# Kernel optimization log

Hardware: AMD Instinct MI355X
Metric: run time of the kernel (lower is better)

The kernel has to match this reference:

```python
import jax, jax.numpy as jnp
import numpy as np

NMS_KS = 15
TOP_K = 2048
GAUSS_KS = 7
GAUSS_SIGMA = 1.0
LOSS_LAMBDA = 1.0


def setup_inputs() -> dict:
    key = jax.random.key(0)
    k1, k2, k3 = jax.random.split(key, 3)
    B, H, W = 16, 1024, 1024
    score1 = jax.random.uniform(k1, (B, 1, H, W), dtype=jnp.float32)
    w_score2 = jax.random.uniform(k2, (B, 1, H, W), dtype=jnp.float32)
    w_vis_mask2 = jax.random.randint(k3, (B, 1, H, W), 0, 2) > 0
    return {"score1": score1, "w_score2": w_score2, "w_vis_mask2": w_vis_mask2}


def _nms(score, ks):
    # keep only local maxima within a ks x ks window (stride 1, 'same' padding)
    pooled = jax.lax.reduce_window(score, -jnp.inf, jax.lax.max,
                                   (1, 1, ks, ks), (1, 1, 1, 1), 'SAME')
    return jnp.where(score == pooled, score, jnp.zeros_like(score))


def _prepare_gt_score(score, nms_ks, k, mask):
    # NMS -> mask -> per-image top-k -> binary GT keypoint map
    s = _nms(score, nms_ks) * mask.astype(score.dtype)
    b = s.shape[0]
    flat = s.reshape(b, -1)                      # B x (H*W)
    _, idx = jax.lax.top_k(flat, k)              # B x k
    gt = jnp.zeros_like(flat).at[jnp.arange(b)[:, None], idx].set(1.0)
    return gt.reshape(s.shape)


def _gaussian_filter(x, ks, sigma):
    coords = jnp.arange(ks, dtype=jnp.float32) - (ks - 1) / 2.0
    g = jnp.exp(-(coords ** 2) / (2.0 * sigma ** 2))
    g = g / g.sum()
    k2d = jnp.outer(g, g)[None, None]
    pad = ks // 2
    return jax.lax.conv_general_dilated(
        x, k2d, (1, 1), [(pad, pad), (pad, pad)],
        dimension_numbers=('NCHW', 'OIHW', 'NCHW'))


def reference(score1, w_score2, w_vis_mask2):
    b = score1.shape[0]
    gt_score1 = jax.lax.stop_gradient(
        _prepare_gt_score(w_score2, NMS_KS, TOP_K, w_vis_mask2))
    gt_score1 = _gaussian_filter(gt_score1, GAUSS_KS, GAUSS_SIGMA)
    m = w_vis_mask2.astype(jnp.float32)
    loss = ((score1 - gt_score1) ** 2) * m       # masked elementwise MSE
    loss = loss.reshape(b, -1).sum(-1) / jnp.clip(m.reshape(b, -1).sum(-1), 1e-8)
    return LOSS_LAMBDA * loss.mean()
```

## Files before the change

### kernel.cpp

```cpp
#include <hip/hip_runtime.h>
#include <math.h>

#define BATCH 16
#define H 1024
#define W 1024
#define NTILES 8192
#define NBANDS (NTILES * 4)
#define CAP 4096
#define TOPK 2048
#define BCW 12

struct WS {
  float pt1[NBANDS];
  int   pmc[NBANDS];
  int   band_cnt[NBANDS];
  float corr_part[BATCH * 64];
  float band_val[NBANDS * BCW];
  int   band_idx[NBANDS * BCW];
};

__constant__ float GW[7] = {
  0.004433048175f, 0.054005582623f, 0.242036229376f, 0.399050279652f,
  0.242036229376f, 0.054005582623f, 0.004433048175f
};

__device__ __forceinline__ float4 max4(float4 a, float4 b) {
  float4 r;
  r.x = fmaxf(a.x, b.x); r.y = fmaxf(a.y, b.y);
  r.z = fmaxf(a.z, b.z); r.w = fmaxf(a.w, b.w);
  return r;
}

__global__ __launch_bounds__(256, 5) void k_nms(const float* __restrict__ score1,
                                                const float* __restrict__ score2,
                                                const int* __restrict__ mask,
                                                WS* __restrict__ ws) {
  __shared__ float4 halo[4][22][21];
  const int tid = threadIdx.x;
  const int w = tid >> 6, l = tid & 63;

  const int t = (blockIdx.x & 7) * (NTILES / 8) + (blockIdx.x >> 3);
  const int b  = t >> 9;
  const int tt = t & 511;
  const int ty0 = (tt >> 4) << 5;
  const int tx0 = (tt & 15) << 6;
  const int by0 = ty0 + (w << 3);
  const size_t ibase = (size_t)b * ((size_t)H * W);
  const float* s2 = score2 + ibase;

  const int rl = l >> 3;
  const int c8 = l & 7;
  const size_t pb = ibase + (size_t)(by0 + rl) * W + tx0 + (c8 << 3);
  const float4 s1a = *(const float4*)(score1 + pb);
  const float4 s1b = *(const float4*)(score1 + pb + 4);
  const int4  mka = *(const int4*)(mask + pb);
  const int4  mkb = *(const int4*)(mask + pb + 4);

  float4 st[7]; int sr[7], sc[7];
  #pragma unroll
  for (int k = 0; k < 7; k++) {
    const int slot = l + (k << 6);
    if (slot < 440) {
      const int r = slot / 20, c = slot - r * 20;
      sr[k] = r; sc[k] = c;
      const int gy = by0 - 7 + r, gx = tx0 - 8 + (c << 2);
      const bool ok = (gy >= 0) & (gy < H) & (gx >= 0) & (gx < W);
      const int gyc = min(max(gy, 0), H - 1);
      const int gxc = ok ? gx : 0;
      float4 v = *(const float4*)(s2 + (size_t)gyc * W + gxc);
      if (!ok) v = make_float4(-INFINITY, -INFINITY, -INFINITY, -INFINITY);
      st[k] = v;
    }
  }

  float t1 = 0.f; int mcnt = 0; unsigned int mbits = 0;
  {
    const float sc_[8] = {s1a.x, s1a.y, s1a.z, s1a.w, s1b.x, s1b.y, s1b.z, s1b.w};
    const int   mm[8] = {mka.x, mka.y, mka.z, mka.w, mkb.x, mkb.y, mkb.z, mkb.w};
    #pragma unroll
    for (int j = 0; j < 8; j++) {
      if (mm[j]) { t1 = fmaf(sc_[j], sc_[j], t1); mcnt++; mbits |= (1u << j); }
    }
  }

  #pragma unroll
  for (int k = 0; k < 7; k++) {
    const int slot = l + (k << 6);
    if (slot < 440) halo[w][sr[k]][sc[k]] = st[k];
  }
  __builtin_amdgcn_wave_barrier();
  asm volatile("s_waitcnt lgkmcnt(0)" ::: "memory");
  __builtin_amdgcn_sched_barrier(0);

  float4 vr0, vr1, vr2, vr3;
  int R0 = 0, cg = 0;
  if (l < 40) {
    const int r2 = l / 20;
    cg = l - r2 * 20;
    R0 = r2 << 2;
    float4 core = halo[w][R0 + 3][cg];
    #pragma unroll
    for (int k = 4; k <= 14; k++) core = max4(core, halo[w][R0 + k][cg]);
    const float4 h0 = halo[w][R0][cg], h1 = halo[w][R0 + 1][cg], h2 = halo[w][R0 + 2][cg];
    const float4 h15 = halo[w][R0 + 15][cg], h16 = halo[w][R0 + 16][cg], h17 = halo[w][R0 + 17][cg];
    const float4 p2 = h2, p1 = max4(h1, p2), p0 = max4(h0, p1);
    const float4 sf15 = h15, sf16 = max4(sf15, h16), sf17 = max4(sf16, h17);
    vr0 = max4(core, p0);
    vr1 = max4(max4(core, p1), sf15);
    vr2 = max4(max4(core, p2), sf16);
    vr3 = max4(core, sf17);
  }
  const float4 cva = halo[w][rl + 7][(c8 << 1) + 2];
  const float4 cvb = halo[w][rl + 7][(c8 << 1) + 3];
  __builtin_amdgcn_wave_barrier();
  asm volatile("s_waitcnt lgkmcnt(0)" ::: "memory");
  __builtin_amdgcn_sched_barrier(0);

  if (l < 40) {
    halo[w][R0 + 0][cg] = vr0;
    halo[w][R0 + 1][cg] = vr1;
    halo[w][R0 + 2][cg] = vr2;
    halo[w][R0 + 3][cg] = vr3;
  }
  __builtin_amdgcn_wave_barrier();
  asm volatile("s_waitcnt lgkmcnt(0)" ::: "memory");
  __builtin_amdgcn_sched_barrier(0);

  float r[24];
  #pragma unroll
  for (int g = 0; g < 6; g++) {
    float4 v = halo[w][rl][(c8 << 1) + g];
    r[4 * g + 0] = v.x; r[4 * g + 1] = v.y; r[4 * g + 2] = v.z; r[4 * g + 3] = v.w;
  }
  float core = r[8];
  #pragma unroll
  for (int k = 9; k <= 15; k++) core = fmaxf(core, r[k]);
  const float q7 = r[7];
  const float q6 = fmaxf(r[6], q7);
  const float q5 = fmaxf(r[5], q6);
  const float q4 = fmaxf(r[4], q5);
  const float q3 = fmaxf(r[3], q4);
  const float q2 = fmaxf(r[2], q3);
  const float q1 = fmaxf(r[1], q2);
  float sa[7];
  sa[0] = r[16];
  #pragma unroll
  for (int k = 1; k < 7; k++) sa[k] = fmaxf(sa[k - 1], r[16 + k]);
  float pooled[8];
  pooled[0] = fmaxf(core, q1);
  pooled[1] = fmaxf(fmaxf(core, q2), sa[0]);
  pooled[2] = fmaxf(fmaxf(core, q3), sa[1]);
  pooled[3] = fmaxf(fmaxf(core, q4), sa[2]);
  pooled[4] = fmaxf(fmaxf(core, q5), sa[3]);
  pooled[5] = fmaxf(fmaxf(core, q6), sa[4]);
  pooled[6] = fmaxf(fmaxf(core, q7), sa[5]);
  pooled[7] = fmaxf(core, sa[6]);

  const float cc[8] = {cva.x, cva.y, cva.z, cva.w, cvb.x, cvb.y, cvb.z, cvb.w};
  int cj = -1; float cv = 0.f;
  #pragma unroll
  for (int j = 0; j < 8; j++) {
    if (((mbits >> j) & 1u) && cj < 0) {
      const float s = cc[j];
      if (s == pooled[j] && s > 0.f) { cj = j; cv = s; }
    }
  }
  const int band = (t << 2) + w;
  const unsigned long long bal = __ballot(cj >= 0);
  if (cj >= 0) {
    const int pos = (int)__popcll(bal & ((1ull << l) - 1ull));
    if (pos < BCW) {
      ws->band_val[band * BCW + pos] = cv;
      ws->band_idx[band * BCW + pos] = (by0 + rl) * W + tx0 + (c8 << 3) + cj;
    }
  }
  #pragma unroll
  for (int off = 32; off > 0; off >>= 1) {
    t1 += __shfl_down(t1, off);
    mcnt += __shfl_down(mcnt, off);
  }
  if (l == 0) {
    int nc = (int)__popcll(bal); if (nc > BCW) nc = BCW;
    ws->band_cnt[band] = nc;
    ws->pt1[band] = t1;
    ws->pmc[band] = mcnt;
  }
}

__global__ __launch_bounds__(256, 4) void k_rankstamp(const float* __restrict__ score1,
                                                      const int* __restrict__ mask,
                                                      WS* __restrict__ ws) {
  const int blk = (blockIdx.x & 7) * 128 + (blockIdx.x >> 3);
  const int b = blk >> 6;
  const int slice = blk & 63;
  __shared__ __align__(16) float sval[CAP];
  __shared__ __align__(16) int   sidx[CAP];
  __shared__ int   wt[4];
  __shared__ int   s_tot;
  __shared__ int   s_prank[4][64];
  __shared__ int   s_keys[64];
  __shared__ int   s_nk;
  __shared__ float cred[4];
  const int tid = threadIdx.x;
  const int w = tid >> 6, l = tid & 63;

  const int base = b * 2048 + tid * 8;
  int c[8]; int csum = 0;
  #pragma unroll
  for (int u = 0; u < 8; u++) {
    int x = ws->band_cnt[base + u];
    if (x > BCW) x = BCW;
    c[u] = x; csum += x;
  }
  int v = csum;
  #pragma unroll
  for (int off = 1; off < 64; off <<= 1) {
    int u2 = __shfl_up(v, off);
    if (l >= off) v += u2;
  }
  if (l == 63) wt[w] = v;
  __syncthreads();
  int wo = 0;
  #pragma unroll
  for (int k = 0; k < 4; k++) if (k < w) wo += wt[k];
  const int excl = v - csum + wo;
  if (tid == 255) {
    int tot = excl + csum;
    if (tot > CAP) tot = CAP;
    s_tot = tot;
    #pragma unroll
    for (int u = 0; u < 3; u++)
      if (tot + u < CAP) sval[tot + u] = 0.f;
  }
  int off = excl;
  #pragma unroll
  for (int u = 0; u < 8; u++) {
    const float* sv = ws->band_val + (size_t)(base + u) * BCW;
    const int*   si = ws->band_idx + (size_t)(base + u) * BCW;
    for (int j = 0; j < c[u]; j++) {
      if (off < CAP) { sval[off] = sv[j]; sidx[off] = si[j]; }
      off++;
    }
  }
  __syncthreads();

  const int n = s_tot;
  const int i0 = slice << 6;
  if (i0 >= n) {
    if (tid == 0) ws->corr_part[b * 64 + slice] = 0.f;
    return;
  }
  const int nf4 = (n + 3) >> 2;

  const float vi = sval[i0 + l];
  const int   xi = sidx[i0 + l];
  const int q = (nf4 + 3) >> 2;
  int lo = w * q; if (lo > nf4) lo = nf4;
  int hi = lo + q; if (hi > nf4) hi = nf4;
  int rank = 0;
  int j = lo;
  for (; j + 4 <= hi; j += 4) {
    #pragma unroll
    for (int u = 0; u < 4; u++) {
      const float4 vv = ((const float4*)sval)[j + u];
      const int4  iv = ((const int4*)sidx)[j + u];
      rank += (vv.x > vi) + (vv.y > vi) + (vv.z > vi) + (vv.w > vi);
      rank += (vv.x == vi && iv.x < xi);
      rank += (vv.y == vi && iv.y < xi);
      rank += (vv.z == vi && iv.z < xi);
      rank += (vv.w == vi && iv.w < xi);
    }
  }
  for (; j < hi; j++) {
    const float4 vv = ((const float4*)sval)[j];
    const int4  iv = ((const int4*)sidx)[j];
    rank += (vv.x > vi) + (vv.y > vi) + (vv.z > vi) + (vv.w > vi);
    rank += (vv.x == vi && iv.x < xi);
    rank += (vv.y == vi && iv.y < xi);
    rank += (vv.z == vi && iv.z < xi);
    rank += (vv.w == vi && iv.w < xi);
  }
  s_prank[w][l] = rank;
  __syncthreads();

  if (tid < 64) {
    const int rtot = s_prank[0][tid] + s_prank[1][tid] + s_prank[2][tid] + s_prank[3][tid];
    const bool sel = (i0 + tid < n) && (rtot < TOPK);
    const unsigned long long bal = __ballot(sel);
    if (sel) {
      const int pos = __popcll(bal & ((1ull << tid) - 1ull));
      s_keys[pos] = sidx[i0 + tid];
    }
    if (tid == 0) s_nk = (int)__popcll(bal);
  }
  __syncthreads();
  const int nk = s_nk;

  float contrib = 0.f;
  const int sub = tid & 7;
  const size_t ib2 = (size_t)b * ((size_t)H * W);
  #pragma unroll
  for (int rnd = 0; rnd < 2; rnd++) {
    const int k = (tid >> 3) + (rnd << 5);
    if (k < nk && sub < 7) {
      const int ck = s_keys[k];
      const int cy = ck >> 10, cx = ck & 1023;
      const int py = cy + sub - 3;
      const float wy = GW[sub] * ((py >= 0 && py < H) ? 1.f : 0.f);
      const int pyc = min(max(py, 0), H - 1);
      const float* s1r = score1 + ib2 + (size_t)pyc * W;
      const int*   mr  = mask   + ib2 + (size_t)pyc * W;
      #pragma unroll
      for (int dx = -3; dx <= 3; dx++) {
        const int px = cx + dx;
        const float wv = wy * GW[dx + 3] * ((px >= 0 && px < W) ? 1.f : 0.f);
        const int pxc = min(max(px, 0), W - 1);
        const float mf = (mr[pxc] != 0) ? 1.f : 0.f;
        contrib += mf * wv * (wv - 2.f * s1r[pxc]);
      }
    }
  }
  #pragma unroll
  for (int off2 = 32; off2 > 0; off2 >>= 1) contrib += __shfl_down(contrib, off2);
  if (l == 0) cred[w] = contrib;
  __syncthreads();
  if (tid == 0)
    ws->corr_part[b * 64 + slice] = (cred[0] + cred[1]) + (cred[2] + cred[3]);
}

__global__ __launch_bounds__(1024) void k_final(WS* __restrict__ ws, float* __restrict__ out) {
  const int tid = threadIdx.x;
  const int b = tid >> 6, l = tid & 63;
  __shared__ double sD[BATCH];

  double tsum = 0.0; long long msum = 0;
  const float4* pv = (const float4*)(ws->pt1 + b * 2048);
  const int4*   pm = (const int4*)(ws->pmc + b * 2048);
  #pragma unroll
  for (int k = 0; k < 8; k++) {
    const float4 f = pv[l + (k << 6)];
    const int4   m = pm[l + (k << 6)];
    tsum += (double)f.x + (double)f.y + (double)f.z + (double)f.w;
    msum += (long long)(m.x + m.y + m.z + m.w);
  }
  double csum = (double)ws->corr_part[b * 64 + l];
  #pragma unroll
  for (int off = 32; off > 0; off >>= 1) {
    tsum += __shfl_down(tsum, off);
    msum += __shfl_down(msum, off);
    csum += __shfl_down(csum, off);
  }
  if (l == 0) {
    double denom = (double)msum;
    if (denom < 1e-8) denom = 1e-8;
    sD[b] = (tsum + csum) / denom;
  }
  __syncthreads();
  if (tid == 0) {
    double acc = 0.0;
    #pragma unroll
    for (int k = 0; k < BATCH; k++) acc += sD[k];
    out[0] = (float)(acc / BATCH);
  }
}

extern "C" void kernel_launch(void* const* d_in, const int* in_sizes, int n_in,
                              void* d_out, int out_size, void* d_ws, size_t ws_size,
                              hipStream_t stream) {
  const float* score1 = (const float*)d_in[0];
  const float* score2 = (const float*)d_in[1];
  const int*   mask   = (const int*)d_in[2];
  float* out = (float*)d_out;
  WS* ws = (WS*)d_ws;

  k_nms<<<NTILES, 256, 0, stream>>>(score1, score2, mask, ws);
  k_rankstamp<<<BATCH * 64, 256, 0, stream>>>(score1, mask, ws);
  k_final<<<1, 1024, 0, stream>>>(ws, out);
}
```

Baseline: 89.76 us.

## Compact per-image candidates once in a separate kernel before rank stamping

Moves the band-count prefix scan and scattered candidate gather out of every rank-stamp block into a new per-image compaction kernel that writes a contiguous candidate list to global memory. Each rank-stamp block then checks its slice against the stored count first, exiting early before touching band data, and otherwise loads the compact list with vectorized float4/int4 copies. This removes 64-fold redundant scanning and gathering per image, at the cost of an extra launch, a tiny 16-block kernel, and an extra global round trip.

```diff
diff --git a/kernel.cpp b/kernel.cpp
--- a/kernel.cpp
+++ b/kernel.cpp
@@ -14,9 +14,12 @@
   float pt1[NBANDS];
   int   pmc[NBANDS];
   int   band_cnt[NBANDS];
+  int   cand_count[BATCH];
   float corr_part[BATCH * 64];
   float band_val[NBANDS * BCW];
   int   band_idx[NBANDS * BCW];
+  float ccand_val[BATCH * CAP];
+  int   ccand_idx[BATCH * CAP];
 };
 
 __constant__ float GW[7] = {
@@ -187,70 +190,83 @@
   }
 }
 
+__global__ __launch_bounds__(256) void k_compact(WS* __restrict__ ws) {
+  const int b = blockIdx.x;
+  const int tid = threadIdx.x;
+  const int lane = tid & 63, w = tid >> 6;
+  __shared__ int wt[4];
+
+  const int base = b * 2048 + tid * 8;
+  int c[8]; int csum = 0;
+  #pragma unroll
+  for (int u = 0; u < 8; u++) {
+    int x = ws->band_cnt[base + u];
+    if (x > BCW) x = BCW;
+    c[u] = x; csum += x;
+  }
+  int v = csum;
+  #pragma unroll
+  for (int off = 1; off < 64; off <<= 1) {
+    int u2 = __shfl_up(v, off);
+    if (lane >= off) v += u2;
+  }
+  if (lane == 63) wt[w] = v;
+  __syncthreads();
+  int wo = 0;
+  #pragma unroll
+  for (int k = 0; k < 4; k++) if (k < w) wo += wt[k];
+  const int excl = v - csum + wo;
+  float* dv = ws->ccand_val + b * CAP;
+  int*   di = ws->ccand_idx + b * CAP;
+  if (tid == 255) {
+    int tot = excl + csum;
+    if (tot > CAP) tot = CAP;
+    ws->cand_count[b] = tot;
+    #pragma unroll
+    for (int u = 0; u < 3; u++)
+      if (tot + u < CAP) dv[tot + u] = 0.f;
+  }
+  int off = excl;
+  #pragma unroll
+  for (int u = 0; u < 8; u++) {
+    const float* sv = ws->band_val + (size_t)(base + u) * BCW;
+    const int*   si = ws->band_idx + (size_t)(base + u) * BCW;
+    for (int j = 0; j < c[u]; j++) {
+      if (off < CAP) { dv[off] = sv[j]; di[off] = si[j]; }
+      off++;
+    }
+  }
+}
+
 __global__ __launch_bounds__(256, 4) void k_rankstamp(const float* __restrict__ score1,
                                                       const int* __restrict__ mask,
                                                       WS* __restrict__ ws) {
   const int blk = (blockIdx.x & 7) * 128 + (blockIdx.x >> 3);
   const int b = blk >> 6;
   const int slice = blk & 63;
+  int n = ws->cand_count[b]; if (n > CAP) n = CAP;
+  const int i0 = slice << 6;
+  if (i0 >= n) {
+    if (threadIdx.x == 0) ws->corr_part[b * 64 + slice] = 0.f;
+    return;
+  }
   __shared__ __align__(16) float sval[CAP];
   __shared__ __align__(16) int   sidx[CAP];
-  __shared__ int   wt[4];
-  __shared__ int   s_tot;
   __shared__ int   s_prank[4][64];
   __shared__ int   s_keys[64];
   __shared__ int   s_nk;
   __shared__ float cred[4];
   const int tid = threadIdx.x;
   const int w = tid >> 6, l = tid & 63;
-
-  const int base = b * 2048 + tid * 8;
-  int c[8]; int csum = 0;
-  #pragma unroll
-  for (int u = 0; u < 8; u++) {
-    int x = ws->band_cnt[base + u];
-    if (x > BCW) x = BCW;
-    c[u] = x; csum += x;
-  }
-  int v = csum;
-  #pragma unroll
-  for (int off = 1; off < 64; off <<= 1) {
-    int u2 = __shfl_up(v, off);
-    if (l >= off) v += u2;
-  }
-  if (l == 63) wt[w] = v;
-  __syncthreads();
-  int wo = 0;
-  #pragma unroll
-  for (int k = 0; k < 4; k++) if (k < w) wo += wt[k];
-  const int excl = v - csum + wo;
-  if (tid == 255) {
-    int tot = excl + csum;
-    if (tot > CAP) tot = CAP;
-    s_tot = tot;
-    #pragma unroll
-    for (int u = 0; u < 3; u++)
-      if (tot + u < CAP) sval[tot + u] = 0.f;
-  }
-  int off = excl;
-  #pragma unroll
-  for (int u = 0; u < 8; u++) {
-    const float* sv = ws->band_val + (size_t)(base + u) * BCW;
-    const int*   si = ws->band_idx + (size_t)(base + u) * BCW;
-    for (int j = 0; j < c[u]; j++) {
-      if (off < CAP) { sval[off] = sv[j]; sidx[off] = si[j]; }
-      off++;
-    }
-  }
-  __syncthreads();
-
-  const int n = s_tot;
-  const int i0 = slice << 6;
-  if (i0 >= n) {
-    if (tid == 0) ws->corr_part[b * 64 + slice] = 0.f;
-    return;
-  }
   const int nf4 = (n + 3) >> 2;
+
+  const float4* gv = (const float4*)(ws->ccand_val + b * CAP);
+  const int4*   gi = (const int4*)(ws->ccand_idx + b * CAP);
+  for (int j = tid; j < nf4; j += 256) {
+    ((float4*)sval)[j] = gv[j];
+    ((int4*)sidx)[j]   = gi[j];
+  }
+  __syncthreads();
 
   const float vi = sval[i0 + l];
   const int   xi = sidx[i0 + l];
@@ -374,6 +390,7 @@
   WS* ws = (WS*)d_ws;
 
   k_nms<<<NTILES, 256, 0, stream>>>(score1, score2, mask, ws);
+  k_compact<<<BATCH, 256, 0, stream>>>(ws);
   k_rankstamp<<<BATCH * 64, 256, 0, stream>>>(score1, mask, ws);
   k_final<<<1, 1024, 0, stream>>>(ws, out);
 }
```

New measurement: 85.65 us. 1.05x faster.
